# Kernel optimization log

Hardware: AMD Instinct MI355X
Metric: run time of the kernel (lower is better)

## Reference

```python
import jax, jax.numpy as jnp
import numpy as np

B, L, D, H = 256, 256, 128, 256
IMPUTE_WEIGHT = 1.0


def setup_inputs() -> dict:
    key = jax.random.key(0)
    ks = jax.random.split(key, 20)
    s = 0.05
    inp = {
        "values": jax.random.normal(ks[0], (B, L, D), jnp.float32),
        "masks": jax.random.randint(ks[1], (B, L, D), 0, 2).astype(jnp.float32),
        "deltas": jax.random.uniform(ks[2], (B, L, D), jnp.float32),
        "eval_masks": jax.random.randint(ks[3], (B, L, D), 0, 2).astype(jnp.float32),
        "td_h_W": jax.random.normal(ks[4], (H, D), jnp.float32) * s,
        "td_h_b": jax.random.normal(ks[5], (H,), jnp.float32) * s,
        "td_x_w": jax.random.normal(ks[6], (D,), jnp.float32) * s,  # diag of TemporalDecay(diag=True)
        "td_x_b": jax.random.normal(ks[7], (D,), jnp.float32) * s,
        "hist_W": jax.random.normal(ks[8], (D, H), jnp.float32) * s,
        "hist_b": jax.random.normal(ks[9], (D,), jnp.float32) * s,
        "feat_W": jax.random.normal(ks[10], (D, D), jnp.float32) * s,
        "feat_b": jax.random.normal(ks[11], (D,), jnp.float32) * s,
        "wc_W": jax.random.normal(ks[12], (D, 2 * D), jnp.float32) * s,
        "wc_b": jax.random.normal(ks[13], (D,), jnp.float32) * s,
        "W_ih": jax.random.normal(ks[14], (4 * H, 2 * D), jnp.float32) * s,
        "W_hh": jax.random.normal(ks[15], (4 * H, H), jnp.float32) * s,
        "b_ih": jax.random.normal(ks[16], (4 * H,), jnp.float32) * s,
        "b_hh": jax.random.normal(ks[17], (4 * H,), jnp.float32) * s,
    }
    return inp


def _rits_forward(values, masks, deltas, eval_masks,
                  td_h_W, td_h_b, td_x_w, td_x_b,
                  hist_W, hist_b, feat_W, feat_b,
                  wc_W, wc_b, W_ih, W_hh, b_ih, b_hh):
    feat_mask = 1.0 - jnp.eye(D, dtype=values.dtype)  # zero diagonal
    Wf = feat_W * feat_mask

    def step(carry, xs):
        h, c, loss = carry
        x, m, d, me = xs  # each (B, D)
        gamma_h = jnp.exp(-jax.nn.relu(d @ td_h_W.T + td_h_b))   # (B, H)
        gamma_x = jnp.exp(-jax.nn.relu(d * td_x_w + td_x_b))      # (B, D) diag linear
        h = h * gamma_h
        x_h = h @ hist_W.T + hist_b                               # (B, D)
        x_c = m * x + (1.0 - m) * x_h
        z_h = x_c @ Wf.T + feat_b                                 # (B, D)
        alpha = jnp.concatenate([gamma_x, m], axis=1) @ wc_W.T + wc_b
        c_h = alpha * z_h + (1.0 - alpha) * x_h
        c_c = m * x + (1.0 - m) * c_h
        loss = loss + jnp.sum(jnp.abs(c_c - x) * me) / (jnp.sum(me) + 1e-5)
        inputs = jnp.concatenate([c_c, m], axis=1)                # (B, 2D)
        gates = inputs @ W_ih.T + b_ih + h @ W_hh.T + b_hh        # (B, 4H)
        i, f, g, o = jnp.split(gates, 4, axis=1)
        i, f, o = jax.nn.sigmoid(i), jax.nn.sigmoid(f), jax.nn.sigmoid(o)
        g = jnp.tanh(g)
        c = f * c + i * g
        h = o * jnp.tanh(c)
        return (h, c, loss), c_c

    h0 = jnp.zeros((values.shape[0], H), values.dtype)
    c0 = jnp.zeros((values.shape[0], H), values.dtype)
    loss0 = jnp.zeros((), values.dtype)
    xs = (jnp.swapaxes(values, 0, 1), jnp.swapaxes(masks, 0, 1),
          jnp.swapaxes(deltas, 0, 1), jnp.swapaxes(eval_masks, 0, 1))  # (L, B, D)
    (_, _, loss), imps = jax.lax.scan(step, (h0, c0, loss0), xs)
    imputations = jnp.swapaxes(imps, 0, 1)  # (B, L, D)
    return imputations, loss * IMPUTE_WEIGHT


def reference(values, masks, deltas, eval_masks,
              td_h_W, td_h_b, td_x_w, td_x_b,
              hist_W, hist_b, feat_W, feat_b,
              wc_W, wc_b, W_ih, W_hh, b_ih, b_hh):
    return _rits_forward(values, masks, deltas, eval_masks,
                         td_h_W, td_h_b, td_x_w, td_x_b,
                         hist_W, hist_b, feat_W, feat_b,
                         wc_W, wc_b, W_ih, W_hh, b_ih, b_hh)
```

## Files before the change

### kernel.cpp

```cpp
#include <hip/hip_runtime.h>
#include <math.h>


namespace {
constexpr int Bn = 256, Ln = 256, Dn = 128, Hn = 256;
constexpr long LD = (long)Ln * Dn;

constexpr int OFF_LOSS  = 0;
constexpr int OFF_DEN   = 256;
constexpr int OFF_BIASG = 2048;
constexpr int OFF_WG    = 8192;
constexpr int OFF_HISTP = 1056768;
constexpr int OFF_TDHP  = 1122304;
constexpr int OFF_WFP   = 1187840;
constexpr int OFF_WCP   = 1220608;
}

typedef _Float16 h2f __attribute__((ext_vector_type(2)));
typedef unsigned int uint32;

__device__ __forceinline__ float fdot2(uint32 a, uint32 b, float c) {
  return __builtin_amdgcn_fdot2(__builtin_bit_cast(h2f, a),
                                __builtin_bit_cast(h2f, b), c, false);
}
__device__ __forceinline__ uint32 packf16(float a, float b) {
  h2f p; p[0] = (_Float16)a; p[1] = (_Float16)b;
  return __builtin_bit_cast(uint32, p);
}
__device__ __forceinline__ unsigned short f16u(float a) {
  _Float16 h = (_Float16)a; return __builtin_bit_cast(unsigned short, h);
}

__global__ void rits_prep(const float* __restrict__ td_h_W,
                          const float* __restrict__ hist_W,
                          const float* __restrict__ feat_W,
                          const float* __restrict__ wc_W,
                          const float* __restrict__ W_ih,
                          const float* __restrict__ W_hh,
                          const float* __restrict__ b_ih,
                          const float* __restrict__ b_hh,
                          const float* __restrict__ evalm,
                          char* __restrict__ wsb) {
  const int blk = blockIdx.x, tid = threadIdx.x;
  if (blk < 1248) {
    int idx = blk * 256 + tid;
    if (idx < 262144) {
      int kp = idx >> 11, rem = idx & 2047, jj = rem >> 3, s8 = rem & 7;
      const float* src = (s8 < 4) ? W_ih : W_hh;
      int q = s8 & 3;
      const float* row = src + (size_t)(q * 256 + jj) * 256 + 2 * kp;
      ((uint32*)(wsb + OFF_WG))[idx] = packf16(row[0], row[1]);
    } else if (idx < 278528) {
      int i2 = idx - 262144, kp = i2 >> 7, d = i2 & 127;
      ((uint32*)(wsb + OFF_HISTP))[i2] =
          packf16(hist_W[d * 256 + 2 * kp], hist_W[d * 256 + 2 * kp + 1]);
    } else if (idx < 294912) {
      int i2 = idx - 278528, kp = i2 >> 8, h = i2 & 255;
      ((uint32*)(wsb + OFF_TDHP))[i2] =
          packf16(td_h_W[h * 128 + 2 * kp], td_h_W[h * 128 + 2 * kp + 1]);
    } else if (idx < 303104) {
      int i2 = idx - 294912, kp = i2 >> 7, d = i2 & 127;
      float a = (2 * kp == d) ? 0.f : feat_W[d * 128 + 2 * kp];
      float b = (2 * kp + 1 == d) ? 0.f : feat_W[d * 128 + 2 * kp + 1];
      ((uint32*)(wsb + OFF_WFP))[i2] = packf16(a, b);
    } else if (idx < 319488) {
      int i2 = idx - 303104, kp = i2 >> 7, d = i2 & 127;
      ((uint32*)(wsb + OFF_WCP))[i2] =
          packf16(wc_W[d * 256 + 2 * kp], wc_W[d * 256 + 2 * kp + 1]);
    }
  } else if (blk < 1252) {
    int i = (blk - 1248) * 256 + tid;
    int jj = i >> 2, q = i & 3;
    ((float*)(wsb + OFF_BIASG))[jj * 4 + q] =
        b_ih[q * 256 + jj] + b_hh[q * 256 + jj];
    if (blk == 1248 && tid == 0) *((float*)(wsb + OFF_LOSS)) = 0.f;
  } else {
    int t = blk - 1252;
    __shared__ float red[256];
    int d = tid & 127, g = tid >> 7;
    float s = 0.f;
    for (int b = g; b < 256; b += 2) s += evalm[(size_t)b * LD + t * 128 + d];
    red[tid] = s;
    __syncthreads();
    for (int o = 128; o > 0; o >>= 1) {
      if (tid < o) red[tid] += red[tid + o];
      __syncthreads();
    }
    if (tid == 0) ((float*)(wsb + OFF_DEN))[t] = red[0] + 1e-5f;
  }
}

__global__ __launch_bounds__(1024, 4) void rits_rec(
    const float* __restrict__ values, const float* __restrict__ masks,
    const float* __restrict__ deltas, const float* __restrict__ evalm,
    const float* __restrict__ td_h_b, const float* __restrict__ td_x_w,
    const float* __restrict__ td_x_b, const float* __restrict__ hist_b,
    const float* __restrict__ feat_b, const float* __restrict__ wc_b,
    char* __restrict__ wsb, float* __restrict__ outp) {
  __shared__ __align__(16) float scratch[8224];
  __shared__ float den_s[256], bg_s[1024], tdhb_s[256];
  __shared__ float txw_s[128], txb_s[128], hb_s[128], fb_s[128], wcb_s[128];
  __shared__ float hf[2][256], cst[2][256];
  __shared__ float xs[2][128], ms[2][128], es[2][128];
  __shared__ float xh_s[2][128], al_s[2][128];
  __shared__ __align__(8) unsigned short hdU16[128 * 4];
  __shared__ __align__(8) unsigned short cmU16[128 * 4];
  __shared__ __align__(8) unsigned short xcU16[64 * 4];
  __shared__ uint32 drP[64 * 2];
  __shared__ uint32 gxmP[128 * 2];

  const int tid = threadIdx.x;
  const size_t b0 = (size_t)blockIdx.x * 2;
  const uint32* hdU32 = (const uint32*)hdU16;
  const uint32* cmU32 = (const uint32*)cmU16;
  const uint32* xcU32 = (const uint32*)xcU16;
  const uint32* wg = (const uint32*)(wsb + OFF_WG);
  const uint4* histP4 = (const uint4*)(wsb + OFF_HISTP);
  const uint4* tdhP4 = (const uint4*)(wsb + OFF_TDHP);
  const uint4* wfP4 = (const uint4*)(wsb + OFF_WFP);
  const uint4* wcP4 = (const uint4*)(wsb + OFF_WCP);

  if (tid < 512) { ((float*)hf)[tid] = 0.f; ((float*)cst)[tid] = 0.f; }
  bg_s[tid] = ((const float*)(wsb + OFF_BIASG))[tid];
  if (tid < 256) {
    den_s[tid] = ((const float*)(wsb + OFF_DEN))[tid];
    tdhb_s[tid] = td_h_b[tid];
  } else if (tid < 384) txw_s[tid - 256] = td_x_w[tid - 256];
  else if (tid < 512) txb_s[tid - 384] = td_x_b[tid - 384];
  else if (tid < 640) hb_s[tid - 512] = hist_b[tid - 512];
  else if (tid < 768) fb_s[tid - 640] = feat_b[tid - 640];
  else if (tid < 896) wcb_s[tid - 768] = wc_b[tid - 768];
  __syncthreads();

  float lacc = 0.f;
  for (int t = 0; t < Ln; ++t) {
    const size_t base = b0 * LD + (size_t)t * 128;
    if (tid < 256) {
      int d = tid & 127, r = tid >> 7;
      size_t gi = base + (size_t)r * LD + d;
      xs[r][d] = values[gi];
      ms[r][d] = masks[gi];
      es[r][d] = evalm[gi];
    } else if (tid < 512) {
      int i = tid - 256, kp = i & 127, r = i >> 7;
      size_t gb = base + (size_t)r * LD;
      if (kp < 64) {
        float d0v = deltas[gb + 2 * kp], d1v = deltas[gb + 2 * kp + 1];
        drP[kp * 2 + r] = packf16(d0v, d1v);
        float g0 = __expf(-fmaxf(fmaf(d0v, txw_s[2 * kp], txb_s[2 * kp]), 0.f));
        float g1 = __expf(-fmaxf(fmaf(d1v, txw_s[2 * kp + 1], txb_s[2 * kp + 1]), 0.f));
        gxmP[kp * 2 + r] = packf16(g0, g1);
      } else {
        int k2 = kp - 64;
        gxmP[kp * 2 + r] = packf16(masks[gb + 2 * k2], masks[gb + 2 * k2 + 1]);
      }
    }
    __syncthreads();

    if (tid < 256) {
      int g = tid & 63, r = (tid >> 6) & 1, kq = tid >> 7;
      float4 a = {0.f, 0.f, 0.f, 0.f};
#pragma unroll 4
      for (int i = 0; i < 32; ++i) {
        int kp = kq * 32 + i;
        uint4 w = tdhP4[kp * 64 + g];
        uint32 dr = drP[kp * 2 + r];
        a.x = fdot2(dr, w.x, a.x); a.y = fdot2(dr, w.y, a.y);
        a.z = fdot2(dr, w.z, a.z); a.w = fdot2(dr, w.w, a.w);
      }
      ((float4*)(scratch + (kq * 2 + r) * 260))[g] = a;
    } else if (tid < 768) {
      int i0 = tid - 256, g = i0 & 31, r = (i0 >> 5) & 1, kq = i0 >> 6;
      float4 a = {0.f, 0.f, 0.f, 0.f};
#pragma unroll 4
      for (int i = 0; i < 16; ++i) {
        int kp = kq * 16 + i;
        uint4 w = wcP4[kp * 32 + g];
        uint32 gm = gxmP[kp * 2 + r];
        a.x = fdot2(gm, w.x, a.x); a.y = fdot2(gm, w.y, a.y);
        a.z = fdot2(gm, w.z, a.z); a.w = fdot2(gm, w.w, a.w);
      }
      ((float4*)(scratch + 1040 + (kq * 2 + r) * 132))[g] = a;
    }
    __syncthreads();

    if (tid < 512) {
      int h = tid & 255, r = tid >> 8;
      float s = scratch[r * 260 + h] + scratch[(2 + r) * 260 + h] + tdhb_s[h];
      float hd = hf[r][h] * __expf(-fmaxf(s, 0.f));
      hdU16[(h >> 1) * 4 + 2 * r + (h & 1)] = f16u(hd);
    } else if (tid < 768) {
      int i0 = tid - 512, d = i0 & 127, r = i0 >> 7;
      float s = wcb_s[d];
#pragma unroll
      for (int kq = 0; kq < 8; ++kq) s += scratch[1040 + (kq * 2 + r) * 132 + d];
      al_s[r][d] = s;
    }
    __syncthreads();

    if (tid < 512) {
      int g = tid & 31, r = (tid >> 5) & 1, kq = tid >> 6;
      float4 a = {0.f, 0.f, 0.f, 0.f};
#pragma unroll 4
      for (int i = 0; i < 16; ++i) {
        int kp = kq * 16 + i;
        uint4 w = histP4[kp * 32 + g];
        uint32 hd = hdU32[kp * 2 + r];
        a.x = fdot2(hd, w.x, a.x); a.y = fdot2(hd, w.y, a.y);
        a.z = fdot2(hd, w.z, a.z); a.w = fdot2(hd, w.w, a.w);
      }
      ((float4*)(scratch + (kq * 2 + r) * 132))[g] = a;
    }
    __syncthreads();

    if (tid < 256) {
      int d = tid & 127, r = tid >> 7;
      float xh = hb_s[d];
#pragma unroll
      for (int kq = 0; kq < 8; ++kq) xh += scratch[(kq * 2 + r) * 132 + d];
      xh_s[r][d] = xh;
      float mm = ms[r][d];
      float xc = mm * xs[r][d] + (1.f - mm) * xh;
      xcU16[(d >> 1) * 4 + 2 * r + (d & 1)] = f16u(xc);
    }
    __syncthreads();

    if (tid < 512) {
      int g = tid & 31, r = (tid >> 5) & 1, kq = tid >> 6;
      float4 a = {0.f, 0.f, 0.f, 0.f};
#pragma unroll 4
      for (int i = 0; i < 8; ++i) {
        int kp = kq * 8 + i;
        uint4 w = wfP4[kp * 32 + g];
        uint32 xc = xcU32[kp * 2 + r];
        a.x = fdot2(xc, w.x, a.x); a.y = fdot2(xc, w.y, a.y);
        a.z = fdot2(xc, w.z, a.z); a.w = fdot2(xc, w.w, a.w);
      }
      ((float4*)(scratch + (kq * 2 + r) * 132))[g] = a;
    }
    __syncthreads();

    if (tid < 256) {
      int d = tid & 127, r = tid >> 7;
      float z = fb_s[d];
#pragma unroll
      for (int kq = 0; kq < 8; ++kq) z += scratch[(kq * 2 + r) * 132 + d];
      float a = al_s[r][d], xh = xh_s[r][d];
      float ch = a * z + (1.f - a) * xh;
      float mm = ms[r][d], xv = xs[r][d];
      float cc = mm * xv + (1.f - mm) * ch;
      outp[base + (size_t)r * LD + d] = cc;
      lacc += (1.f - mm) * fabsf(ch - xv) * es[r][d] / den_s[t];
      cmU16[(d >> 1) * 4 + 2 * r + (d & 1)] = f16u(cc);
      cmU16[(64 + (d >> 1)) * 4 + 2 * r + (d & 1)] = f16u(mm);
    }
    __syncthreads();

    {
      int jj = tid & 255, kq = tid >> 8;
      int kp0 = kq * 32;
      const uint4* wp = (const uint4*)(wg + ((size_t)kp0 * 256 + jj) * 8);
      float a00 = 0, a01 = 0, a02 = 0, a03 = 0;
      float a10 = 0, a11 = 0, a12 = 0, a13 = 0;
#pragma unroll 4
      for (int i = 0; i < 32; ++i) {
        int kp = kp0 + i;
        uint4 wv = wp[0];
        uint4 wh = wp[1];
        wp += 512;
        uint32 c0 = cmU32[kp * 2 + 0], c1 = cmU32[kp * 2 + 1];
        uint32 h0 = hdU32[kp * 2 + 0], h1 = hdU32[kp * 2 + 1];
        a00 = fdot2(c0, wv.x, a00); a01 = fdot2(c0, wv.y, a01);
        a02 = fdot2(c0, wv.z, a02); a03 = fdot2(c0, wv.w, a03);
        a10 = fdot2(c1, wv.x, a10); a11 = fdot2(c1, wv.y, a11);
        a12 = fdot2(c1, wv.z, a12); a13 = fdot2(c1, wv.w, a13);
        a00 = fdot2(h0, wh.x, a00); a01 = fdot2(h0, wh.y, a01);
        a02 = fdot2(h0, wh.z, a02); a03 = fdot2(h0, wh.w, a03);
        a10 = fdot2(h1, wh.x, a10); a11 = fdot2(h1, wh.y, a11);
        a12 = fdot2(h1, wh.z, a12); a13 = fdot2(h1, wh.w, a13);
      }
      float* pg = scratch;
      pg[(kq * 8 + 0) * 257 + jj] = a00; pg[(kq * 8 + 1) * 257 + jj] = a01;
      pg[(kq * 8 + 2) * 257 + jj] = a02; pg[(kq * 8 + 3) * 257 + jj] = a03;
      pg[(kq * 8 + 4) * 257 + jj] = a10; pg[(kq * 8 + 5) * 257 + jj] = a11;
      pg[(kq * 8 + 6) * 257 + jj] = a12; pg[(kq * 8 + 7) * 257 + jj] = a13;
    }
    __syncthreads();

    if (tid < 256) {
      int jj = tid;
      const float* pg = scratch;
#pragma unroll
      for (int r = 0; r < 2; ++r) {
        float g0 = bg_s[jj * 4 + 0], g1 = bg_s[jj * 4 + 1];
        float g2 = bg_s[jj * 4 + 2], g3 = bg_s[jj * 4 + 3];
#pragma unroll
        for (int kq = 0; kq < 4; ++kq) {
          g0 += pg[(kq * 8 + r * 4 + 0) * 257 + jj];
          g1 += pg[(kq * 8 + r * 4 + 1) * 257 + jj];
          g2 += pg[(kq * 8 + r * 4 + 2) * 257 + jj];
          g3 += pg[(kq * 8 + r * 4 + 3) * 257 + jj];
        }
        float ig = 1.f / (1.f + __expf(-g0));
        float fg = 1.f / (1.f + __expf(-g1));
        float gg = tanhf(g2);
        float og = 1.f / (1.f + __expf(-g3));
        float c = fg * cst[r][jj] + ig * gg;
        cst[r][jj] = c;
        hf[r][jj] = og * tanhf(c);
      }
    }
    __syncthreads();
  }

  scratch[tid] = lacc;
  __syncthreads();
  for (int o = 512; o > 0; o >>= 1) {
    if (tid < o) scratch[tid] += scratch[tid + o];
    __syncthreads();
  }
  if (tid == 0) atomicAdd((float*)(wsb + OFF_LOSS), scratch[0]);
}

__global__ void rits_fin(const char* __restrict__ wsb, float* __restrict__ outp) {
  if (threadIdx.x == 0 && blockIdx.x == 0)
    outp[(size_t)Bn * LD] = *((const float*)(wsb + OFF_LOSS));
}

extern "C" void kernel_launch(void* const* d_in, const int* in_sizes, int n_in,
                              void* d_out, int out_size, void* d_ws,
                              size_t ws_size, hipStream_t stream) {
  const float* values = (const float*)d_in[0];
  const float* masks  = (const float*)d_in[1];
  const float* deltas = (const float*)d_in[2];
  const float* evalm  = (const float*)d_in[3];
  const float* td_h_W = (const float*)d_in[4];
  const float* td_h_b = (const float*)d_in[5];
  const float* td_x_w = (const float*)d_in[6];
  const float* td_x_b = (const float*)d_in[7];
  const float* hist_W = (const float*)d_in[8];
  const float* hist_b = (const float*)d_in[9];
  const float* feat_W = (const float*)d_in[10];
  const float* feat_b = (const float*)d_in[11];
  const float* wc_W   = (const float*)d_in[12];
  const float* wc_b   = (const float*)d_in[13];
  const float* W_ih   = (const float*)d_in[14];
  const float* W_hh   = (const float*)d_in[15];
  const float* b_ih   = (const float*)d_in[16];
  const float* b_hh   = (const float*)d_in[17];
  char* wsb = (char*)d_ws;
  float* outp = (float*)d_out;

  hipLaunchKernelGGL(rits_prep, dim3(1508), dim3(256), 0, stream, td_h_W,
                     hist_W, feat_W, wc_W, W_ih, W_hh, b_ih, b_hh, evalm, wsb);
  hipLaunchKernelGGL(rits_rec, dim3(128), dim3(1024), 0, stream, values, masks,
                     deltas, evalm, td_h_b, td_x_w, td_x_b, hist_b, feat_b,
                     wc_b, wsb, outp);
  hipLaunchKernelGGL(rits_fin, dim3(1), dim3(64), 0, stream, wsb, outp);
}
```

Baseline: 3.540 ms.

## Quantize LSTM gate weights and activations to int8 with sdot4 accumulation

The W_ih/W_hh gate weights are prepacked as int8 with per-column, per-half scales instead of fp16, and the gate matvec switches from fdot2 to 4-way int8 sdot4 with integer accumulators. The imputed input c_c gets a per-step dynamic scale from a wave max-reduction. The mask is stored exactly as int8, and the decayed hidden state is quantized with a fixed 1/127 scale. This halves the weight bytes streamed every timestep and doubles MACs per instruction. In exchange it adds an extra barrier and reduction per step and brings int8 rounding error into the recurrence, which may accumulate over 256 steps.

```diff
diff --git a/kernel.cpp b/kernel.cpp
--- a/kernel.cpp
+++ b/kernel.cpp
@@ -9,11 +9,15 @@
 constexpr int OFF_LOSS  = 0;
 constexpr int OFF_DEN   = 256;
 constexpr int OFF_BIASG = 2048;
-constexpr int OFF_WG    = 8192;
-constexpr int OFF_HISTP = 1056768;
-constexpr int OFF_TDHP  = 1122304;
-constexpr int OFF_WFP   = 1187840;
-constexpr int OFF_WCP   = 1220608;
+constexpr int OFF_SW    = 8192;
+constexpr int OFF_WQ8   = 24576;
+constexpr int OFF_HISTP = 548864;
+constexpr int OFF_TDHP  = 614400;
+constexpr int OFF_WFP   = 679936;
+constexpr int OFF_WCP   = 712704;
+
+constexpr int DSM_FLOATS = 8224 + 4096;
+constexpr int DSM_BYTES  = DSM_FLOATS * 4;
 }
 
 typedef _Float16 h2f __attribute__((ext_vector_type(2)));
@@ -22,6 +26,9 @@
 __device__ __forceinline__ float fdot2(uint32 a, uint32 b, float c) {
   return __builtin_amdgcn_fdot2(__builtin_bit_cast(h2f, a),
                                 __builtin_bit_cast(h2f, b), c, false);
+}
+__device__ __forceinline__ int sdot4(uint32 a, uint32 b, int c) {
+  return __builtin_amdgcn_sdot4((int)a, (int)b, c, false);
 }
 __device__ __forceinline__ uint32 packf16(float a, float b) {
   h2f p; p[0] = (_Float16)a; p[1] = (_Float16)b;
@@ -42,40 +49,58 @@
                           const float* __restrict__ evalm,
                           char* __restrict__ wsb) {
   const int blk = blockIdx.x, tid = threadIdx.x;
-  if (blk < 1248) {
-    int idx = blk * 256 + tid;
-    if (idx < 262144) {
-      int kp = idx >> 11, rem = idx & 2047, jj = rem >> 3, s8 = rem & 7;
-      const float* src = (s8 < 4) ? W_ih : W_hh;
-      int q = s8 & 3;
-      const float* row = src + (size_t)(q * 256 + jj) * 256 + 2 * kp;
-      ((uint32*)(wsb + OFF_WG))[idx] = packf16(row[0], row[1]);
-    } else if (idx < 278528) {
-      int i2 = idx - 262144, kp = i2 >> 7, d = i2 & 127;
-      ((uint32*)(wsb + OFF_HISTP))[i2] =
-          packf16(hist_W[d * 256 + 2 * kp], hist_W[d * 256 + 2 * kp + 1]);
-    } else if (idx < 294912) {
-      int i2 = idx - 278528, kp = i2 >> 8, h = i2 & 255;
-      ((uint32*)(wsb + OFF_TDHP))[i2] =
-          packf16(td_h_W[h * 128 + 2 * kp], td_h_W[h * 128 + 2 * kp + 1]);
-    } else if (idx < 303104) {
-      int i2 = idx - 294912, kp = i2 >> 7, d = i2 & 127;
-      float a = (2 * kp == d) ? 0.f : feat_W[d * 128 + 2 * kp];
-      float b = (2 * kp + 1 == d) ? 0.f : feat_W[d * 128 + 2 * kp + 1];
-      ((uint32*)(wsb + OFF_WFP))[i2] = packf16(a, b);
-    } else if (idx < 319488) {
-      int i2 = idx - 303104, kp = i2 >> 7, d = i2 & 127;
-      ((uint32*)(wsb + OFF_WCP))[i2] =
-          packf16(wc_W[d * 256 + 2 * kp], wc_W[d * 256 + 2 * kp + 1]);
-    }
-  } else if (blk < 1252) {
-    int i = (blk - 1248) * 256 + tid;
+  if (blk < 16) {
+    int task = blk * 256 + tid;
+    int s = task >> 10, col = task & 1023;
+    int q = col >> 8, jj = col & 255;
+    const float* src = ((s < 2) ? W_ih : W_hh) + (size_t)col * 256 + (s & 1) * 128;
+    float mx = 0.f;
+    for (int k = 0; k < 128; k += 4) {
+      float4 v = *(const float4*)(src + k);
+      mx = fmaxf(mx, fmaxf(fmaxf(fabsf(v.x), fabsf(v.y)),
+                           fmaxf(fabsf(v.z), fabsf(v.w))));
+    }
+    float inv = mx > 0.f ? 127.f / mx : 0.f;
+    ((float*)(wsb + OFF_SW))[s * 1024 + col] = mx / 127.f;
+    for (int k16 = 0; k16 < 8; ++k16) {
+      uint32 dw[4];
+      for (int d4 = 0; d4 < 4; ++d4) {
+        uint32 v = 0;
+        for (int j = 0; j < 4; ++j) {
+          int qv = __float2int_rn(src[k16 * 16 + d4 * 4 + j] * inv);
+          qv = qv < -127 ? -127 : (qv > 127 ? 127 : qv);
+          v |= ((uint32)(qv & 0xff)) << (8 * j);
+        }
+        dw[d4] = v;
+      }
+      uint4 u = {dw[0], dw[1], dw[2], dw[3]};
+      ((uint4*)(wsb + OFF_WQ8))[((s * 8 + k16) * 4 + q) * 256 + jj] = u;
+    }
+  } else if (blk < 80) {
+    int i2 = (blk - 16) * 256 + tid, kp = i2 >> 7, d = i2 & 127;
+    ((uint32*)(wsb + OFF_HISTP))[i2] =
+        packf16(hist_W[d * 256 + 2 * kp], hist_W[d * 256 + 2 * kp + 1]);
+  } else if (blk < 144) {
+    int i2 = (blk - 80) * 256 + tid, kp = i2 >> 8, h = i2 & 255;
+    ((uint32*)(wsb + OFF_TDHP))[i2] =
+        packf16(td_h_W[h * 128 + 2 * kp], td_h_W[h * 128 + 2 * kp + 1]);
+  } else if (blk < 176) {
+    int i2 = (blk - 144) * 256 + tid, kp = i2 >> 7, d = i2 & 127;
+    float a = (2 * kp == d) ? 0.f : feat_W[d * 128 + 2 * kp];
+    float b = (2 * kp + 1 == d) ? 0.f : feat_W[d * 128 + 2 * kp + 1];
+    ((uint32*)(wsb + OFF_WFP))[i2] = packf16(a, b);
+  } else if (blk < 240) {
+    int i2 = (blk - 176) * 256 + tid, kp = i2 >> 7, d = i2 & 127;
+    ((uint32*)(wsb + OFF_WCP))[i2] =
+        packf16(wc_W[d * 256 + 2 * kp], wc_W[d * 256 + 2 * kp + 1]);
+  } else if (blk < 244) {
+    int i = (blk - 240) * 256 + tid;
     int jj = i >> 2, q = i & 3;
     ((float*)(wsb + OFF_BIASG))[jj * 4 + q] =
         b_ih[q * 256 + jj] + b_hh[q * 256 + jj];
-    if (blk == 1248 && tid == 0) *((float*)(wsb + OFF_LOSS)) = 0.f;
+    if (blk == 240 && tid == 0) *((float*)(wsb + OFF_LOSS)) = 0.f;
   } else {
-    int t = blk - 1252;
+    int t = blk - 244;
     __shared__ float red[256];
     int d = tid & 127, g = tid >> 7;
     float s = 0.f;
@@ -89,6 +114,8 @@
     if (tid == 0) ((float*)(wsb + OFF_DEN))[t] = red[0] + 1e-5f;
   }
 }
+
+extern __shared__ __align__(16) char dsm[];
 
 __global__ __launch_bounds__(1024, 4) void rits_rec(
     const float* __restrict__ values, const float* __restrict__ masks,
@@ -97,31 +124,39 @@
     const float* __restrict__ td_x_b, const float* __restrict__ hist_b,
     const float* __restrict__ feat_b, const float* __restrict__ wc_b,
     char* __restrict__ wsb, float* __restrict__ outp) {
-  __shared__ __align__(16) float scratch[8224];
+  float* scratch = (float*)dsm;
+  int* scratchI = (int*)dsm;
+  float* sw_s = scratch + 8224;
+
   __shared__ float den_s[256], bg_s[1024], tdhb_s[256];
   __shared__ float txw_s[128], txb_s[128], hb_s[128], fb_s[128], wcb_s[128];
   __shared__ float hf[2][256], cst[2][256];
   __shared__ float xs[2][128], ms[2][128], es[2][128];
   __shared__ float xh_s[2][128], al_s[2][128];
   __shared__ __align__(8) unsigned short hdU16[128 * 4];
-  __shared__ __align__(8) unsigned short cmU16[128 * 4];
   __shared__ __align__(8) unsigned short xcU16[64 * 4];
   __shared__ uint32 drP[64 * 2];
   __shared__ uint32 gxmP[128 * 2];
+  __shared__ __align__(16) uint4 cc8u4[2][8];
+  __shared__ __align__(16) uint4 m8u4[2][8];
+  __shared__ __align__(16) uint4 hd8u4[2][16];
+  __shared__ float s_cc_s;
 
   const int tid = threadIdx.x;
   const size_t b0 = (size_t)blockIdx.x * 2;
   const uint32* hdU32 = (const uint32*)hdU16;
-  const uint32* cmU32 = (const uint32*)cmU16;
   const uint32* xcU32 = (const uint32*)xcU16;
-  const uint32* wg = (const uint32*)(wsb + OFF_WG);
   const uint4* histP4 = (const uint4*)(wsb + OFF_HISTP);
   const uint4* tdhP4 = (const uint4*)(wsb + OFF_TDHP);
   const uint4* wfP4 = (const uint4*)(wsb + OFF_WFP);
   const uint4* wcP4 = (const uint4*)(wsb + OFF_WCP);
+  const uint4* wq8 = (const uint4*)(wsb + OFF_WQ8);
 
   if (tid < 512) { ((float*)hf)[tid] = 0.f; ((float*)cst)[tid] = 0.f; }
   bg_s[tid] = ((const float*)(wsb + OFF_BIASG))[tid];
+#pragma unroll
+  for (int i = 0; i < 4; ++i)
+    sw_s[tid + i * 1024] = ((const float*)(wsb + OFF_SW))[tid + i * 1024];
   if (tid < 256) {
     den_s[tid] = ((const float*)(wsb + OFF_DEN))[tid];
     tdhb_s[tid] = td_h_b[tid];
@@ -135,12 +170,15 @@
   float lacc = 0.f;
   for (int t = 0; t < Ln; ++t) {
     const size_t base = b0 * LD + (size_t)t * 128;
+    float cc_reg = 0.f;
     if (tid < 256) {
       int d = tid & 127, r = tid >> 7;
       size_t gi = base + (size_t)r * LD + d;
-      xs[r][d] = values[gi];
-      ms[r][d] = masks[gi];
+      float vv = values[gi], mm = masks[gi];
+      xs[r][d] = vv;
+      ms[r][d] = mm;
       es[r][d] = evalm[gi];
+      ((signed char*)m8u4)[r * 128 + d] = (signed char)mm;
     } else if (tid < 512) {
       int i = tid - 256, kp = i & 127, r = i >> 7;
       size_t gb = base + (size_t)r * LD;
@@ -189,6 +227,7 @@
       float s = scratch[r * 260 + h] + scratch[(2 + r) * 260 + h] + tdhb_s[h];
       float hd = hf[r][h] * __expf(-fmaxf(s, 0.f));
       hdU16[(h >> 1) * 4 + 2 * r + (h & 1)] = f16u(hd);
+      ((signed char*)hd8u4)[r * 256 + h] = (signed char)__float2int_rn(hd * 127.f);
     } else if (tid < 768) {
       int i0 = tid - 512, d = i0 & 127, r = i0 >> 7;
       float s = wcb_s[d];
@@ -251,60 +290,72 @@
       float cc = mm * xv + (1.f - mm) * ch;
       outp[base + (size_t)r * LD + d] = cc;
       lacc += (1.f - mm) * fabsf(ch - xv) * es[r][d] / den_s[t];
-      cmU16[(d >> 1) * 4 + 2 * r + (d & 1)] = f16u(cc);
-      cmU16[(64 + (d >> 1)) * 4 + 2 * r + (d & 1)] = f16u(mm);
+      cc_reg = cc;
+      float am = fabsf(cc);
+#pragma unroll
+      for (int off = 32; off > 0; off >>= 1) am = fmaxf(am, __shfl_xor(am, off));
+      if ((tid & 63) == 0) scratch[8208 + (tid >> 6)] = am;
+    }
+    __syncthreads();
+
+    if (tid < 256) {
+      int d = tid & 127, r = tid >> 7;
+      float mx = fmaxf(fmaxf(scratch[8208], scratch[8209]),
+                       fmaxf(scratch[8210], scratch[8211]));
+      float inv = mx > 0.f ? 127.f / mx : 0.f;
+      if (tid == 0) s_cc_s = mx / 127.f;
+      float v = fminf(fmaxf(cc_reg * inv, -127.f), 127.f);
+      ((signed char*)cc8u4)[r * 128 + d] = (signed char)__float2int_rn(v);
     }
     __syncthreads();
 
     {
-      int jj = tid & 255, kq = tid >> 8;
-      int kp0 = kq * 32;
-      const uint4* wp = (const uint4*)(wg + ((size_t)kp0 * 256 + jj) * 8);
-      float a00 = 0, a01 = 0, a02 = 0, a03 = 0;
-      float a10 = 0, a11 = 0, a12 = 0, a13 = 0;
-#pragma unroll 4
-      for (int i = 0; i < 32; ++i) {
-        int kp = kp0 + i;
-        uint4 wv = wp[0];
-        uint4 wh = wp[1];
-        wp += 512;
-        uint32 c0 = cmU32[kp * 2 + 0], c1 = cmU32[kp * 2 + 1];
-        uint32 h0 = hdU32[kp * 2 + 0], h1 = hdU32[kp * 2 + 1];
-        a00 = fdot2(c0, wv.x, a00); a01 = fdot2(c0, wv.y, a01);
-        a02 = fdot2(c0, wv.z, a02); a03 = fdot2(c0, wv.w, a03);
-        a10 = fdot2(c1, wv.x, a10); a11 = fdot2(c1, wv.y, a11);
-        a12 = fdot2(c1, wv.z, a12); a13 = fdot2(c1, wv.w, a13);
-        a00 = fdot2(h0, wh.x, a00); a01 = fdot2(h0, wh.y, a01);
-        a02 = fdot2(h0, wh.z, a02); a03 = fdot2(h0, wh.w, a03);
-        a10 = fdot2(h1, wh.x, a10); a11 = fdot2(h1, wh.y, a11);
-        a12 = fdot2(h1, wh.z, a12); a13 = fdot2(h1, wh.w, a13);
-      }
-      float* pg = scratch;
-      pg[(kq * 8 + 0) * 257 + jj] = a00; pg[(kq * 8 + 1) * 257 + jj] = a01;
-      pg[(kq * 8 + 2) * 257 + jj] = a02; pg[(kq * 8 + 3) * 257 + jj] = a03;
-      pg[(kq * 8 + 4) * 257 + jj] = a10; pg[(kq * 8 + 5) * 257 + jj] = a11;
-      pg[(kq * 8 + 6) * 257 + jj] = a12; pg[(kq * 8 + 7) * 257 + jj] = a13;
+      int jj = tid & 255, s = tid >> 8;
+      const uint4* wp = wq8 + (size_t)s * 8192 + jj;
+      const uint4* a0p;
+      const uint4* a1p;
+      if (s == 0) { a0p = cc8u4[0]; a1p = cc8u4[1]; }
+      else if (s == 1) { a0p = m8u4[0]; a1p = m8u4[1]; }
+      else { a0p = hd8u4[0] + (s - 2) * 8; a1p = hd8u4[1] + (s - 2) * 8; }
+      int acc[8] = {0, 0, 0, 0, 0, 0, 0, 0};
+#pragma unroll
+      for (int k16 = 0; k16 < 8; ++k16) {
+        uint4 a0 = a0p[k16], a1 = a1p[k16];
+#pragma unroll
+        for (int q = 0; q < 4; ++q) {
+          uint4 w = wp[k16 * 1024 + q * 256];
+          acc[q * 2 + 0] = sdot4(w.w, a0.w, sdot4(w.z, a0.z,
+                           sdot4(w.y, a0.y, sdot4(w.x, a0.x, acc[q * 2 + 0]))));
+          acc[q * 2 + 1] = sdot4(w.w, a1.w, sdot4(w.z, a1.z,
+                           sdot4(w.y, a1.y, sdot4(w.x, a1.x, acc[q * 2 + 1]))));
+        }
+      }
+#pragma unroll
+      for (int i = 0; i < 8; ++i) scratchI[(s * 8 + i) * 257 + jj] = acc[i];
     }
     __syncthreads();
 
     if (tid < 256) {
       int jj = tid;
-      const float* pg = scratch;
+      float scc = s_cc_s;
+      const float inv127 = 1.f / 127.f;
 #pragma unroll
       for (int r = 0; r < 2; ++r) {
-        float g0 = bg_s[jj * 4 + 0], g1 = bg_s[jj * 4 + 1];
-        float g2 = bg_s[jj * 4 + 2], g3 = bg_s[jj * 4 + 3];
-#pragma unroll
-        for (int kq = 0; kq < 4; ++kq) {
-          g0 += pg[(kq * 8 + r * 4 + 0) * 257 + jj];
-          g1 += pg[(kq * 8 + r * 4 + 1) * 257 + jj];
-          g2 += pg[(kq * 8 + r * 4 + 2) * 257 + jj];
-          g3 += pg[(kq * 8 + r * 4 + 3) * 257 + jj];
+        float gq[4];
+#pragma unroll
+        for (int q = 0; q < 4; ++q) {
+          int col = q * 256 + jj;
+          float a0 = (float)scratchI[(0 * 8 + q * 2 + r) * 257 + jj];
+          float a1 = (float)scratchI[(1 * 8 + q * 2 + r) * 257 + jj];
+          float a2 = (float)scratchI[(2 * 8 + q * 2 + r) * 257 + jj];
+          float a3 = (float)scratchI[(3 * 8 + q * 2 + r) * 257 + jj];
+          gq[q] = bg_s[jj * 4 + q] + scc * sw_s[col] * a0 + sw_s[1024 + col] * a1 +
+                  inv127 * (sw_s[2048 + col] * a2 + sw_s[3072 + col] * a3);
         }
-        float ig = 1.f / (1.f + __expf(-g0));
-        float fg = 1.f / (1.f + __expf(-g1));
-        float gg = tanhf(g2);
-        float og = 1.f / (1.f + __expf(-g3));
+        float ig = 1.f / (1.f + __expf(-gq[0]));
+        float fg = 1.f / (1.f + __expf(-gq[1]));
+        float gg = tanhf(gq[2]);
+        float og = 1.f / (1.f + __expf(-gq[3]));
         float c = fg * cst[r][jj] + ig * gg;
         cst[r][jj] = c;
         hf[r][jj] = og * tanhf(c);
@@ -351,10 +402,12 @@
   char* wsb = (char*)d_ws;
   float* outp = (float*)d_out;
 
-  hipLaunchKernelGGL(rits_prep, dim3(1508), dim3(256), 0, stream, td_h_W,
+  hipFuncSetAttribute((const void*)rits_rec,
+                      hipFuncAttributeMaxDynamicSharedMemorySize, DSM_BYTES);
+  hipLaunchKernelGGL(rits_prep, dim3(500), dim3(256), 0, stream, td_h_W,
                      hist_W, feat_W, wc_W, W_ih, W_hh, b_ih, b_hh, evalm, wsb);
-  hipLaunchKernelGGL(rits_rec, dim3(128), dim3(1024), 0, stream, values, masks,
-                     deltas, evalm, td_h_b, td_x_w, td_x_b, hist_b, feat_b,
-                     wc_b, wsb, outp);
+  hipLaunchKernelGGL(rits_rec, dim3(128), dim3(1024), DSM_BYTES, stream,
+                     values, masks, deltas, evalm, td_h_b, td_x_w, td_x_b,
+                     hist_b, feat_b, wc_b, wsb, outp);
   hipLaunchKernelGGL(rits_fin, dim3(1), dim3(64), 0, stream, wsb, outp);
 }
```

After: 5.024 ms. 41.9% more time.
